# Kernel tuning notes

Hardware: AMD Instinct MI355X
Metric: run time of the kernel (lower is better)

The kernel has to match this reference:

```python
import jax, jax.numpy as jnp
import numpy as np
import math

CHANNELS = 512
OUT_CHANNELS = 512
N_HEADS = 8
WINDOW = 4
K_CH = CHANNELS // N_HEADS


def _conv1x1(x, W, b):
    # x: (B, C_in, T), W: (C_out, C_in), b: (C_out,)
    return jnp.einsum('oc,bct->bot', W, x) + b[None, :, None]


def _get_relative_embeddings(emb, length, window=WINDOW):
    # emb: (H, 2*window+1, k_ch) -> (H, 2*length-1, k_ch)
    pad_length = max(length - (window + 1), 0)
    start = max(window + 1 - length, 0)
    e = jnp.pad(emb, ((0, 0), (pad_length, pad_length), (0, 0))) if pad_length > 0 else emb
    return e[:, start:start + 2 * length - 1]


def _relative_to_absolute(x):
    # x: (B, H, L, 2L-1) -> (B, H, L, L)
    b, h, L, _ = x.shape
    x = jnp.pad(x, ((0, 0), (0, 0), (0, 0), (0, 1)))          # (B,H,L,2L)
    xf = x.reshape(b, h, L * 2 * L)
    xf = jnp.pad(xf, ((0, 0), (0, 0), (L - 1, 0)))
    return xf.reshape(b, h, L + 1, 2 * L - 1)[:, :, :L, L - 1:]


def _absolute_to_relative(x):
    # x: (B, H, L, L) -> (B, H, L, 2L-1)
    b, h, L, _ = x.shape
    x = jnp.pad(x, ((0, 0), (0, 0), (0, 0), (0, L - 1)))       # (B,H,L,2L-1)
    xf = x.reshape(b, h, L * (2 * L - 1))
    xf = jnp.pad(xf, ((0, 0), (0, 0), (L, 0)))
    return xf.reshape(b, h, L, 2 * L)[:, :, :, 1:]


def setup_inputs() -> dict:
    key = jax.random.key(0)
    ks = jax.random.split(key, 16)
    B, C, T = 4, CHANNELS, 1024
    xavier = math.sqrt(2.0 / (C + C))
    rel_std = K_CH ** -0.5
    return {
        'x_q': jax.random.normal(ks[0], (B, C, T), jnp.float32),
        'x_k': jax.random.normal(ks[1], (B, C, T), jnp.float32),
        'x_v': jax.random.normal(ks[2], (B, C, T), jnp.float32),
        'Wq': jax.random.normal(ks[3], (C, C), jnp.float32) * xavier,
        'bq': jnp.zeros((C,), jnp.float32),
        'Wk': jax.random.normal(ks[4], (C, C), jnp.float32) * xavier,
        'bk': jnp.zeros((C,), jnp.float32),
        'Wv': jax.random.normal(ks[5], (C, C), jnp.float32) * xavier,
        'bv': jnp.zeros((C,), jnp.float32),
        'Wo': jax.random.normal(ks[6], (OUT_CHANNELS, C), jnp.float32) * xavier,
        'bo': jnp.zeros((OUT_CHANNELS,), jnp.float32),
        'emb_rel_k': jax.random.normal(ks[7], (N_HEADS, 2 * WINDOW + 1, K_CH), jnp.float32) * rel_std,
        'emb_rel_v': jax.random.normal(ks[8], (N_HEADS, 2 * WINDOW + 1, K_CH), jnp.float32) * rel_std,
    }


def reference(x_q, x_k, x_v, Wq, bq, Wk, bk, Wv, bv, Wo, bo, emb_rel_k, emb_rel_v):
    q = _conv1x1(x_q, Wq, bq)
    k = _conv1x1(x_k, Wk, bk)
    v = _conv1x1(x_v, Wv, bv)
    B, C, T = q.shape
    # (B, C, T) -> (B, H, T, k_ch); head h owns contiguous k_ch channel chunk
    qh = q.reshape(B, N_HEADS, K_CH, T).transpose(0, 1, 3, 2) / math.sqrt(K_CH)
    kh = k.reshape(B, N_HEADS, K_CH, T).transpose(0, 1, 3, 2)
    vh = v.reshape(B, N_HEADS, K_CH, T).transpose(0, 1, 3, 2)
    scores = jnp.einsum('bhtd,bhsd->bhts', qh, kh)              # (B,H,T,T)
    rel_k = _get_relative_embeddings(emb_rel_k, T)              # (H,2T-1,d)
    rel_logits = jnp.einsum('bhtd,hmd->bhtm', qh, rel_k)        # (B,H,T,2T-1)
    scores = scores + _relative_to_absolute(rel_logits)
    attn = jax.nn.softmax(scores, axis=-1)
    ctx = jnp.einsum('bhts,bhsd->bhtd', attn, vh)
    rel_w = _absolute_to_relative(attn)                         # (B,H,T,2T-1)
    rel_v = _get_relative_embeddings(emb_rel_v, T)
    ctx = ctx + jnp.einsum('bhtm,hmd->bhtd', rel_w, rel_v)
    out = ctx.transpose(0, 1, 3, 2).reshape(B, C, T)
    return _conv1x1(out, Wo, bo)
```

## Files before the change

kernel.cpp:

```cpp
#include <hip/hip_runtime.h>

#define T_LEN 1024
#define NH 8
#define DH 64
#define CCH 512
#define LOG2E 1.44269504088896340736f

typedef _Float16 f16;
typedef _Float16 f16x8 __attribute__((ext_vector_type(8)));
typedef _Float16 f16x4 __attribute__((ext_vector_type(4)));
typedef float f32x4 __attribute__((ext_vector_type(4)));

__device__ __forceinline__ void dma16(const void* g, void* l)
{
    __builtin_amdgcn_global_load_lds((const __attribute__((address_space(1))) void*)g,
                                     (__attribute__((address_space(3))) void*)l, 16, 0, 0);
}

__global__ __launch_bounds__(256)
void prep_kernel(const float* __restrict__ x0, const float* __restrict__ x1,
                 const float* __restrict__ x2, const float* __restrict__ W0,
                 const float* __restrict__ W1, const float* __restrict__ W2,
                 const float* __restrict__ W3, f16* __restrict__ o0,
                 f16* __restrict__ o1, f16* __restrict__ o2, f16* __restrict__ w0,
                 f16* __restrict__ w1, f16* __restrict__ w2, f16* __restrict__ w3,
                 int B)
{
    const int z = blockIdx.z;
    if (z < 3 * B) {
        const int t0 = blockIdx.x * 64, c0 = blockIdx.y * 64;
        const int which = z / B, b = z % B;
        const float* x = (which == 0) ? x0 : (which == 1) ? x1 : x2;
        f16* o = (which == 0) ? o0 : (which == 1) ? o1 : o2;

        __shared__ float L[64 * 68];
        const int cl = threadIdx.x & 63, g = threadIdx.x >> 6;
        const float* src = x + ((size_t)(b * CCH + c0 + cl)) * T_LEN + t0 + g * 16;
        #pragma unroll
        for (int j = 0; j < 4; ++j)
            *(float4*)&L[cl * 68 + g * 16 + 4 * j] = *(const float4*)&src[4 * j];
        __syncthreads();
        const int tl = threadIdx.x & 63, cg = (threadIdx.x >> 6) * 16;
        f16 h[16];
        #pragma unroll
        for (int j = 0; j < 16; ++j) h[j] = (f16)L[(cg + j) * 68 + tl];
        f16* dst = o + ((size_t)(b * T_LEN + t0 + tl)) * CCH + c0 + cg;
        *(f16x8*)&dst[0] = *(f16x8*)&h[0];
        *(f16x8*)&dst[8] = *(f16x8*)&h[8];
    } else {
        const int slice = z - 3 * B;
        size_t i = ((size_t)(slice * 128 + blockIdx.y * 16 + blockIdx.x) * 256 + threadIdx.x) * 4;
        const int wi = (int)(i >> 18);
        const size_t off = i & 262143;
        const float* src = (wi == 0) ? W0 : (wi == 1) ? W1 : (wi == 2) ? W2 : W3;
        f16* dst = (wi == 0) ? w0 : (wi == 1) ? w1 : (wi == 2) ? w2 : w3;
        float4 v4 = *(const float4*)&src[off];
        f16x4 h = {(f16)v4.x, (f16)v4.y, (f16)v4.z, (f16)v4.w};
        *(f16x4*)&dst[off] = h;
    }
}

__global__ __launch_bounds__(256)
void proj_qkv(const f16* __restrict__ xq, const f16* __restrict__ xk,
              const f16* __restrict__ xv, const f16* __restrict__ wq,
              const f16* __restrict__ wk, const f16* __restrict__ wv,
              const float* __restrict__ bq, const float* __restrict__ bk,
              const float* __restrict__ bv, f16* __restrict__ qo,
              f16* __restrict__ ko, f16* __restrict__ vo)
{
    const int which = blockIdx.z;
    const f16* X = (which == 0) ? xq : (which == 1) ? xk : xv;
    const f16* W = (which == 0) ? wq : (which == 1) ? wk : wv;
    const float* bias = (which == 0) ? bq : (which == 1) ? bk : bv;
    const float scale = (which == 0) ? 0.125f * LOG2E : 1.0f;

    const int r0 = blockIdx.x * 64;
    const int o0 = blockIdx.y * 64;
    const int tid = threadIdx.x;
    const int w = tid >> 6, quad = (tid >> 4) & 3, l15 = tid & 15;

    __shared__ f16 Xs[64 * 72], Ws[64 * 72];
    f32x4 acc[4] = {};

    for (int c0 = 0; c0 < CCH; c0 += 64) {
        if (c0) __syncthreads();
        #pragma unroll
        for (int j = 0; j < 2; ++j) {
            int cid = tid + 256 * j;
            int row = cid >> 3, c8 = (cid & 7) * 8;
            *(f16x8*)&Xs[row * 72 + c8] = *(const f16x8*)&X[(size_t)(r0 + row) * CCH + c0 + c8];
            *(f16x8*)&Ws[row * 72 + c8] = *(const f16x8*)&W[(size_t)(o0 + row) * CCH + c0 + c8];
        }
        __syncthreads();
        const f16* Ab = (which < 2) ? Xs : Ws;
        const f16* Bb = (which < 2) ? Ws : Xs;
        #pragma unroll
        for (int ks = 0; ks < 2; ++ks) {
            f16x8 a = *(const f16x8*)&Ab[(16 * w + l15) * 72 + ks * 32 + quad * 8];
            #pragma unroll
            for (int ct = 0; ct < 4; ++ct) {
                f16x8 bf = *(const f16x8*)&Bb[(16 * ct + l15) * 72 + ks * 32 + quad * 8];
                acc[ct] = __builtin_amdgcn_mfma_f32_16x16x32_f16(a, bf, acc[ct], 0, 0, 0);
            }
        }
    }

    if (which < 2) {
        f16* out = (which == 0) ? qo : ko;
        #pragma unroll
        for (int ct = 0; ct < 4; ++ct) {
            int col = o0 + 16 * ct + l15;
            float bvl = bias[col];
            #pragma unroll
            for (int r = 0; r < 4; ++r) {
                int row = r0 + 16 * w + quad * 4 + r;
                out[(size_t)row * CCH + col] = (f16)((acc[ct][r] + bvl) * scale);
            }
        }
    } else {
        const int bb = r0 >> 10, tb = r0 & 1023;
        #pragma unroll
        for (int r = 0; r < 4; ++r) {
            int row_o = o0 + 16 * w + quad * 4 + r;
            float bvl = bias[row_o];
            #pragma unroll
            for (int ct = 0; ct < 4; ++ct)
                vo[((size_t)(bb * CCH + row_o)) * T_LEN + tb + 16 * ct + l15] =
                    (f16)(acc[ct][r] + bvl);
        }
    }
}

__global__ __launch_bounds__(256)
void attn_mfma(const f16* __restrict__ q, const f16* __restrict__ kk,
               const f16* __restrict__ v, const float* __restrict__ ekg,
               const float* __restrict__ evg, f16* __restrict__ Op0,
               f16* __restrict__ Op1, float* __restrict__ l0,
               float* __restrict__ l1)
{
    const int t0 = blockIdx.x * 64, h = blockIdx.y;
    const int b = blockIdx.z >> 1, split = blockIdx.z & 1;
    const int tid = threadIdx.x;
    const int w = tid >> 6, lane = tid & 63;
    const int quad = lane >> 4, l15 = lane & 15;

    f16* Op = split ? Op1 : Op0;
    float* lbuf = split ? l1 : l0;

    __shared__ __align__(16) f16 Qs[4096], Ks[4096], Vs[4096], Ps[4096];
    __shared__ float eks[576], evs[576];

    const int srow = tid >> 3;
    const int scol = ((tid & 7) ^ (srow & 7)) << 3;

    for (int i = tid; i < 576; i += 256) {
        eks[i] = ekg[h * 576 + i];
        evs[i] = evg[h * 576 + i];
    }

    dma16(q + ((size_t)(b * T_LEN + t0 + srow)) * CCH + h * DH + scol, &Qs[(size_t)tid * 8]);
    dma16(q + ((size_t)(b * T_LEN + t0 + srow + 32)) * CCH + h * DH + scol, &Qs[((size_t)tid + 256) * 8]);
    __syncthreads();

    f16x8 qf[2];
    #pragma unroll
    for (int ks = 0; ks < 2; ++ks)
        qf[ks] = *(const f16x8*)&Qs[(16 * w + l15) * 64 + (((ks * 4 + quad) ^ (l15 & 7)) << 3)];

    const int kb0 = split * 8;
    const f16* gk = kk + ((size_t)(b * T_LEN + kb0 * 64 + srow)) * CCH + h * DH + scol;
    const f16* gv = v + ((size_t)(b * CCH + h * DH + srow)) * T_LEN + kb0 * 64 + scol;

    const int myt = 16 * w + l15;
    float Ssum = 0.f;
    f32x4 O[4] = {};

    const bool corner_hi = (blockIdx.x == 0) && (split == 1);
    const bool corner_lo = (blockIdx.x == 15) && (split == 0);

    for (int kb = kb0; kb < kb0 + 8; ++kb) {
        __syncthreads();
        dma16(gk, &Ks[(size_t)tid * 8]);
        dma16(gk + (size_t)32 * CCH, &Ks[((size_t)tid + 256) * 8]);
        dma16(gv, &Vs[(size_t)tid * 8]);
        dma16(gv + (size_t)32 * T_LEN, &Vs[((size_t)tid + 256) * 8]);
        gk += (size_t)64 * CCH;
        gv += 64;
        __syncthreads();

        f32x4 S[4] = {};
        #pragma unroll
        for (int ks = 0; ks < 2; ++ks) {
            #pragma unroll
            for (int ct = 0; ct < 4; ++ct) {
                f16x8 a = *(const f16x8*)&Ks[(16 * ct + l15) * 64 + (((ks * 4 + quad) ^ (l15 & 7)) << 3)];
                S[ct] = __builtin_amdgcn_mfma_f32_16x16x32_f16(a, qf[ks], S[ct], 0, 0, 0);
            }
        }

        if ((corner_hi && kb == 15) || (corner_lo && kb == 0)) {
            const int s0g = kb * 64;
            #pragma unroll
            for (int ct = 0; ct < 4; ++ct)
                #pragma unroll
                for (int r = 0; r < 4; ++r) {
                    int t_g = t0 + myt;
                    int s_g = s0g + 16 * ct + 4 * quad + r;
                    int df = s_g - t_g;
                    if (df >= 1019 && df <= 1023) {
                        const float* ekp = &eks[(df - 1019) * 64];
                        float sacc = 0.f;
                        for (int d = 0; d < 64; ++d)
                            sacc += (float)Qs[myt * 64 + (((d >> 3) ^ (myt & 7)) << 3) + (d & 7)] * ekp[d];
                        S[ct][r] += sacc;
                    } else if (df >= -1023 && df <= -1021) {
                        const float* ekp = &eks[(1029 + df) * 64];
                        const int t2 = myt - 1;
                        float sacc = 0.f;
                        for (int d = 0; d < 64; ++d)
                            sacc += (float)Qs[t2 * 64 + (((d >> 3) ^ (t2 & 7)) << 3) + (d & 7)] * ekp[d];
                        S[ct][r] += sacc;
                    }
                }
        }

        #pragma unroll
        for (int ct = 0; ct < 4; ++ct) {
            f16x4 pk_;
            #pragma unroll
            for (int r = 0; r < 4; ++r) {
                float p = exp2f(S[ct][r]);
                Ssum += p;
                pk_[r] = (f16)p;
            }
            int colh = (((2 * ct + (quad >> 1)) ^ (myt & 7)) << 3) + (quad & 1) * 4;
            *(f16x4*)&Ps[myt * 64 + colh] = pk_;
        }
        __syncthreads();

        #pragma unroll
        for (int ks = 0; ks < 2; ++ks) {
            f16x8 a = *(const f16x8*)&Ps[(16 * w + l15) * 64 + (((ks * 4 + quad) ^ (l15 & 7)) << 3)];
            #pragma unroll
            for (int ct = 0; ct < 4; ++ct) {
                f16x8 bf = *(const f16x8*)&Vs[(16 * ct + l15) * 64 + (((ks * 4 + quad) ^ (l15 & 7)) << 3)];
                O[ct] = __builtin_amdgcn_mfma_f32_16x16x32_f16(a, bf, O[ct], 0, 0, 0);
            }
        }

        const int s0g = kb * 64;
        if (s0g <= t0 + 67 && s0g + 63 >= t0 - 4) {
            #pragma unroll
            for (int r = 0; r < 4; ++r) {
                int t_loc = 16 * w + 4 * quad + r;
                int t_g = t0 + t_loc;
                int slo = max(s0g, t_g - 4), shi = min(s0g + 63, t_g + 4);
                for (int s = slo; s <= shi; ++s) {
                    int sl = s - s0g;
                    float p = (float)Ps[t_loc * 64 + (((sl >> 3) ^ (t_loc & 7)) << 3) + (sl & 7)];
                    const float* evp = &evs[(s - t_g + 4) * 64];
                    #pragma unroll
                    for (int ct = 0; ct < 4; ++ct)
                        O[ct][r] += p * evp[16 * ct + l15];
                }
            }
        }
    }

    Ssum += __shfl_xor(Ssum, 16);
    Ssum += __shfl_xor(Ssum, 32);
    if (quad == 0)
        lbuf[((size_t)b * NH + h) * T_LEN + t0 + myt] = Ssum;

    #pragma unroll
    for (int r = 0; r < 4; ++r) {
        int t_g = t0 + 16 * w + 4 * quad + r;
        size_t rowo = ((size_t)(b * T_LEN + t_g)) * CCH + h * DH;
        #pragma unroll
        for (int ct = 0; ct < 4; ++ct)
            Op[rowo + 16 * ct + l15] = (f16)O[ct][r];
    }
}

__global__ __launch_bounds__(256)
void proj_out(const f16* __restrict__ Op0, const f16* __restrict__ Op1,
              const float* __restrict__ l0, const float* __restrict__ l1,
              const f16* __restrict__ Wo, const float* __restrict__ bo,
              float* __restrict__ out)
{
    const int r0 = blockIdx.x * 64;
    const int o0 = blockIdx.y * 64;
    const int tid = threadIdx.x;
    const int w = tid >> 6, quad = (tid >> 4) & 3, l15 = tid & 15;

    __shared__ f16 Xs[64 * 72], Ws[64 * 72];
    f32x4 acc[4] = {};

    for (int c0 = 0; c0 < CCH; c0 += 64) {
        if (c0) __syncthreads();
        #pragma unroll
        for (int j = 0; j < 2; ++j) {
            int cid = tid + 256 * j;
            int rw = cid >> 3, cc = (cid & 7) * 8;
            int gr = r0 + rw;
            int bb = gr >> 10, tt = gr & 1023;
            int hh = (c0 + cc) >> 6;
            size_t li = ((size_t)bb * NH + hh) * T_LEN + tt;
            float rl = 1.0f / (l0[li] + l1[li]);
            f16x8 a0 = *(const f16x8*)&Op0[(size_t)gr * CCH + c0 + cc];
            f16x8 a1 = *(const f16x8*)&Op1[(size_t)gr * CCH + c0 + cc];
            f16 hx[8];
            #pragma unroll
            for (int e = 0; e < 8; ++e)
                hx[e] = (f16)(((float)a0[e] + (float)a1[e]) * rl);
            *(f16x8*)&Xs[rw * 72 + cc] = *(f16x8*)hx;
            *(f16x8*)&Ws[rw * 72 + cc] = *(const f16x8*)&Wo[(size_t)(o0 + rw) * CCH + c0 + cc];
        }
        __syncthreads();
        #pragma unroll
        for (int ks = 0; ks < 2; ++ks) {
            f16x8 a = *(const f16x8*)&Ws[(16 * w + l15) * 72 + ks * 32 + quad * 8];
            #pragma unroll
            for (int ct = 0; ct < 4; ++ct) {
                f16x8 bf = *(const f16x8*)&Xs[(16 * ct + l15) * 72 + ks * 32 + quad * 8];
                acc[ct] = __builtin_amdgcn_mfma_f32_16x16x32_f16(a, bf, acc[ct], 0, 0, 0);
            }
        }
    }

    const int bb = r0 >> 10, tb = r0 & 1023;
    #pragma unroll
    for (int r = 0; r < 4; ++r) {
        int row_o = o0 + 16 * w + quad * 4 + r;
        float bvl = bo[row_o];
        #pragma unroll
        for (int ct = 0; ct < 4; ++ct)
            out[((size_t)(bb * CCH + row_o)) * T_LEN + tb + 16 * ct + l15] =
                acc[ct][r] + bvl;
    }
}

extern "C" void kernel_launch(void* const* d_in, const int* in_sizes, int n_in,
                              void* d_out, int out_size, void* d_ws, size_t ws_size,
                              hipStream_t stream)
{
    const float* x_q = (const float*)d_in[0];
    const float* x_k = (const float*)d_in[1];
    const float* x_v = (const float*)d_in[2];
    const float* Wq  = (const float*)d_in[3];
    const float* bq  = (const float*)d_in[4];
    const float* Wk  = (const float*)d_in[5];
    const float* bk  = (const float*)d_in[6];
    const float* Wv  = (const float*)d_in[7];
    const float* bv  = (const float*)d_in[8];
    const float* Wo  = (const float*)d_in[9];
    const float* bo  = (const float*)d_in[10];
    const float* erk = (const float*)d_in[11];
    const float* erv = (const float*)d_in[12];

    const int B = in_sizes[0] / (CCH * T_LEN);
    const size_t te = (size_t)B * CCH * T_LEN;
    const size_t we = (size_t)CCH * CCH;

    f16* p = (f16*)d_ws;
    f16* xTq = p; p += te;
    f16* xTk = p; p += te;
    f16* xTv = p; p += te;
    f16* wqh = p; p += we;
    f16* wkh = p; p += we;
    f16* wvh = p; p += we;
    f16* woh = p; p += we;
    f16* qh  = p; p += te;
    f16* kh  = p; p += te;
    f16* vh  = p; p += te;

    f16* Op0 = xTq;
    f16* Op1 = xTk;
    float* l0 = (float*)xTv;
    float* l1 = l0 + (size_t)B * NH * T_LEN;

    dim3 blk(256);
    prep_kernel<<<dim3(16, 8, 3 * B + 8), blk, 0, stream>>>(
        x_q, x_k, x_v, Wq, Wk, Wv, Wo, xTq, xTk, xTv, wqh, wkh, wvh, woh, B);
    proj_qkv<<<dim3(B * 16, 8, 3), blk, 0, stream>>>(
        xTq, xTk, xTv, wqh, wkh, wvh, bq, bk, bv, qh, kh, vh);
    attn_mfma<<<dim3(T_LEN / 64, NH, 2 * B), blk, 0, stream>>>(
        qh, kh, vh, erk, erv, Op0, Op1, l0, l1);
    proj_out<<<dim3(B * 16, 8), blk, 0, stream>>>(
        Op0, Op1, l0, l1, woh, bo, (float*)d_out);
}
```

Baseline: 166.4 us.

## Double-buffer projection GEMMs with async LDS DMA, swizzle, and split combine kernel

Both projection GEMMs move to 128x64 tiles with double-buffered shared memory filled by global_load_lds DMA and an XOR swizzle in place of padding, so the next K-chunk loads while MFMAs run. The split-softmax combine (sum of the two partial outputs and normalisation) moves out of proj_out into its own elementwise kernel that writes a normalised context buffer, which lets proj_out use plain DMA loads. This adds one launch and an extra read/write of the context tensor, plus new workspace buffers instead of reusing the input scratch. Doubling the rows per tile halves the grid, which may reduce occupancy.

After: 159.8 us. -4.0%, faster.

```diff
diff --git a/kernel.cpp b/kernel.cpp
--- a/kernel.cpp
+++ b/kernel.cpp
@@ -74,59 +74,99 @@
     const float* bias = (which == 0) ? bq : (which == 1) ? bk : bv;
     const float scale = (which == 0) ? 0.125f * LOG2E : 1.0f;
 
-    const int r0 = blockIdx.x * 64;
+    const int r0 = blockIdx.x * 128;
     const int o0 = blockIdx.y * 64;
     const int tid = threadIdx.x;
-    const int w = tid >> 6, quad = (tid >> 4) & 3, l15 = tid & 15;
-
-    __shared__ f16 Xs[64 * 72], Ws[64 * 72];
-    f32x4 acc[4] = {};
-
-    for (int c0 = 0; c0 < CCH; c0 += 64) {
-        if (c0) __syncthreads();
-        #pragma unroll
-        for (int j = 0; j < 2; ++j) {
-            int cid = tid + 256 * j;
-            int row = cid >> 3, c8 = (cid & 7) * 8;
-            *(f16x8*)&Xs[row * 72 + c8] = *(const f16x8*)&X[(size_t)(r0 + row) * CCH + c0 + c8];
-            *(f16x8*)&Ws[row * 72 + c8] = *(const f16x8*)&W[(size_t)(o0 + row) * CCH + c0 + c8];
-        }
-        __syncthreads();
-        const f16* Ab = (which < 2) ? Xs : Ws;
-        const f16* Bb = (which < 2) ? Ws : Xs;
+    const int w = tid >> 6, lane = tid & 63;
+    const int quad = lane >> 4, l15 = lane & 15;
+
+    __shared__ __align__(16) f16 Xs[2][128 * 64];
+    __shared__ __align__(16) f16 Ws[2][64 * 64];
+
+    const int srow = tid >> 3;
+    const int scol = ((tid & 7) ^ (srow & 7)) << 3;
+
+    const f16* Xg = X + (size_t)(r0 + srow) * CCH + scol;
+    const f16* Wg = W + (size_t)(o0 + srow) * CCH + scol;
+
+    #pragma unroll
+    for (int j = 0; j < 4; ++j)
+        dma16(Xg + (size_t)(32 * j) * CCH, &Xs[0][(size_t)tid * 8 + j * 2048]);
+    #pragma unroll
+    for (int j = 0; j < 2; ++j)
+        dma16(Wg + (size_t)(32 * j) * CCH, &Ws[0][(size_t)tid * 8 + j * 2048]);
+
+    f32x4 acc[8] = {};
+
+    for (int kc = 0; kc < 8; ++kc) {
+        __syncthreads();
+        if (kc < 7) {
+            const int bf = (kc + 1) & 1, c1 = (kc + 1) * 64;
+            #pragma unroll
+            for (int j = 0; j < 4; ++j)
+                dma16(Xg + c1 + (size_t)(32 * j) * CCH, &Xs[bf][(size_t)tid * 8 + j * 2048]);
+            #pragma unroll
+            for (int j = 0; j < 2; ++j)
+                dma16(Wg + c1 + (size_t)(32 * j) * CCH, &Ws[bf][(size_t)tid * 8 + j * 2048]);
+        }
+        const int cb = kc & 1;
         #pragma unroll
         for (int ks = 0; ks < 2; ++ks) {
-            f16x8 a = *(const f16x8*)&Ab[(16 * w + l15) * 72 + ks * 32 + quad * 8];
-            #pragma unroll
-            for (int ct = 0; ct < 4; ++ct) {
-                f16x8 bf = *(const f16x8*)&Bb[(16 * ct + l15) * 72 + ks * 32 + quad * 8];
-                acc[ct] = __builtin_amdgcn_mfma_f32_16x16x32_f16(a, bf, acc[ct], 0, 0, 0);
+            const int sl = ((ks * 4 + quad) ^ (l15 & 7)) << 3;
+            f16x8 xf[2], wf[4];
+            #pragma unroll
+            for (int im = 0; im < 2; ++im)
+                xf[im] = *(const f16x8*)&Xs[cb][(32 * w + 16 * im + l15) * 64 + sl];
+            #pragma unroll
+            for (int cm = 0; cm < 4; ++cm)
+                wf[cm] = *(const f16x8*)&Ws[cb][(16 * cm + l15) * 64 + sl];
+            if (which < 2) {
+                #pragma unroll
+                for (int im = 0; im < 2; ++im)
+                    #pragma unroll
+                    for (int cm = 0; cm < 4; ++cm)
+                        acc[im * 4 + cm] = __builtin_amdgcn_mfma_f32_16x16x32_f16(
+                            xf[im], wf[cm], acc[im * 4 + cm], 0, 0, 0);
+            } else {
+                #pragma unroll
+                for (int cm = 0; cm < 4; ++cm)
+                    #pragma unroll
+                    for (int in = 0; in < 2; ++in)
+                        acc[cm * 2 + in] = __builtin_amdgcn_mfma_f32_16x16x32_f16(
+                            wf[cm], xf[in], acc[cm * 2 + in], 0, 0, 0);
             }
         }
     }
 
     if (which < 2) {
         f16* out = (which == 0) ? qo : ko;
-        #pragma unroll
-        for (int ct = 0; ct < 4; ++ct) {
-            int col = o0 + 16 * ct + l15;
-            float bvl = bias[col];
+        float bl[4];
+        #pragma unroll
+        for (int cm = 0; cm < 4; ++cm) bl[cm] = bias[o0 + 16 * cm + l15];
+        #pragma unroll
+        for (int im = 0; im < 2; ++im)
             #pragma unroll
             for (int r = 0; r < 4; ++r) {
-                int row = r0 + 16 * w + quad * 4 + r;
-                out[(size_t)row * CCH + col] = (f16)((acc[ct][r] + bvl) * scale);
-            }
-        }
+                size_t row = (size_t)(r0 + 32 * w + 16 * im + 4 * quad + r) * CCH;
+                #pragma unroll
+                for (int cm = 0; cm < 4; ++cm)
+                    out[row + o0 + 16 * cm + l15] =
+                        (f16)((acc[im * 4 + cm][r] + bl[cm]) * scale);
+            }
     } else {
         const int bb = r0 >> 10, tb = r0 & 1023;
         #pragma unroll
-        for (int r = 0; r < 4; ++r) {
-            int row_o = o0 + 16 * w + quad * 4 + r;
-            float bvl = bias[row_o];
-            #pragma unroll
-            for (int ct = 0; ct < 4; ++ct)
-                vo[((size_t)(bb * CCH + row_o)) * T_LEN + tb + 16 * ct + l15] =
-                    (f16)(acc[ct][r] + bvl);
+        for (int cm = 0; cm < 4; ++cm) {
+            float4 bv4 = *(const float4*)&bias[o0 + 16 * cm + 4 * quad];
+            float bl[4] = {bv4.x, bv4.y, bv4.z, bv4.w};
+            #pragma unroll
+            for (int r = 0; r < 4; ++r) {
+                size_t row = ((size_t)(bb * CCH + o0 + 16 * cm + 4 * quad + r)) * T_LEN;
+                #pragma unroll
+                for (int in = 0; in < 2; ++in)
+                    vo[row + tb + 32 * w + 16 * in + l15] =
+                        (f16)(acc[cm * 2 + in][r] + bl[r]);
+            }
         }
     }
 }
@@ -283,60 +323,95 @@
 }
 
 __global__ __launch_bounds__(256)
-void proj_out(const f16* __restrict__ Op0, const f16* __restrict__ Op1,
-              const float* __restrict__ l0, const float* __restrict__ l1,
-              const f16* __restrict__ Wo, const float* __restrict__ bo,
-              float* __restrict__ out)
-{
-    const int r0 = blockIdx.x * 64;
+void combine_kernel(const f16* __restrict__ Op0, const f16* __restrict__ Op1,
+                    const float* __restrict__ l0, const float* __restrict__ l1,
+                    f16* __restrict__ ctx)
+{
+    const size_t i8 = ((size_t)blockIdx.x * 256 + threadIdx.x) * 8;
+    const size_t gr = i8 >> 9;
+    const int h = (int)((i8 & 511) >> 6);
+    const size_t li = ((gr >> 10) * NH + h) * T_LEN + (gr & 1023);
+    const float rl = 1.0f / (l0[li] + l1[li]);
+    f16x8 a0 = *(const f16x8*)&Op0[i8];
+    f16x8 a1 = *(const f16x8*)&Op1[i8];
+    f16 o[8];
+    #pragma unroll
+    for (int e = 0; e < 8; ++e)
+        o[e] = (f16)(((float)a0[e] + (float)a1[e]) * rl);
+    *(f16x8*)&ctx[i8] = *(f16x8*)o;
+}
+
+__global__ __launch_bounds__(256)
+void proj_out(const f16* __restrict__ ctx, const f16* __restrict__ Wo,
+              const float* __restrict__ bo, float* __restrict__ out)
+{
+    const int r0 = blockIdx.x * 128;
     const int o0 = blockIdx.y * 64;
     const int tid = threadIdx.x;
-    const int w = tid >> 6, quad = (tid >> 4) & 3, l15 = tid & 15;
-
-    __shared__ f16 Xs[64 * 72], Ws[64 * 72];
-    f32x4 acc[4] = {};
-
-    for (int c0 = 0; c0 < CCH; c0 += 64) {
-        if (c0) __syncthreads();
-        #pragma unroll
-        for (int j = 0; j < 2; ++j) {
-            int cid = tid + 256 * j;
-            int rw = cid >> 3, cc = (cid & 7) * 8;
-            int gr = r0 + rw;
-            int bb = gr >> 10, tt = gr & 1023;
-            int hh = (c0 + cc) >> 6;
-            size_t li = ((size_t)bb * NH + hh) * T_LEN + tt;
-            float rl = 1.0f / (l0[li] + l1[li]);
-            f16x8 a0 = *(const f16x8*)&Op0[(size_t)gr * CCH + c0 + cc];
-            f16x8 a1 = *(const f16x8*)&Op1[(size_t)gr * CCH + c0 + cc];
-            f16 hx[8];
-            #pragma unroll
-            for (int e = 0; e < 8; ++e)
-                hx[e] = (f16)(((float)a0[e] + (float)a1[e]) * rl);
-            *(f16x8*)&Xs[rw * 72 + cc] = *(f16x8*)hx;
-            *(f16x8*)&Ws[rw * 72 + cc] = *(const f16x8*)&Wo[(size_t)(o0 + rw) * CCH + c0 + cc];
-        }
-        __syncthreads();
+    const int w = tid >> 6, lane = tid & 63;
+    const int quad = lane >> 4, l15 = lane & 15;
+
+    __shared__ __align__(16) f16 Cs[2][128 * 64];
+    __shared__ __align__(16) f16 Ws[2][64 * 64];
+
+    const int srow = tid >> 3;
+    const int scol = ((tid & 7) ^ (srow & 7)) << 3;
+
+    const f16* Cg = ctx + (size_t)(r0 + srow) * CCH + scol;
+    const f16* Wg = Wo + (size_t)(o0 + srow) * CCH + scol;
+
+    #pragma unroll
+    for (int j = 0; j < 4; ++j)
+        dma16(Cg + (size_t)(32 * j) * CCH, &Cs[0][(size_t)tid * 8 + j * 2048]);
+    #pragma unroll
+    for (int j = 0; j < 2; ++j)
+        dma16(Wg + (size_t)(32 * j) * CCH, &Ws[0][(size_t)tid * 8 + j * 2048]);
+
+    f32x4 acc[8] = {};
+
+    for (int kc = 0; kc < 8; ++kc) {
+        __syncthreads();
+        if (kc < 7) {
+            const int bf = (kc + 1) & 1, c1 = (kc + 1) * 64;
+            #pragma unroll
+            for (int j = 0; j < 4; ++j)
+                dma16(Cg + c1 + (size_t)(32 * j) * CCH, &Cs[bf][(size_t)tid * 8 + j * 2048]);
+            #pragma unroll
+            for (int j = 0; j < 2; ++j)
+                dma16(Wg + c1 + (size_t)(32 * j) * CCH, &Ws[bf][(size_t)tid * 8 + j * 2048]);
+        }
+        const int cb = kc & 1;
         #pragma unroll
         for (int ks = 0; ks < 2; ++ks) {
-            f16x8 a = *(const f16x8*)&Ws[(16 * w + l15) * 72 + ks * 32 + quad * 8];
-            #pragma unroll
-            for (int ct = 0; ct < 4; ++ct) {
-                f16x8 bf = *(const f16x8*)&Xs[(16 * ct + l15) * 72 + ks * 32 + quad * 8];
-                acc[ct] = __builtin_amdgcn_mfma_f32_16x16x32_f16(a, bf, acc[ct], 0, 0, 0);
-            }
+            const int sl = ((ks * 4 + quad) ^ (l15 & 7)) << 3;
+            f16x8 cf[2], wf[4];
+            #pragma unroll
+            for (int in = 0; in < 2; ++in)
+                cf[in] = *(const f16x8*)&Cs[cb][(32 * w + 16 * in + l15) * 64 + sl];
+            #pragma unroll
+            for (int cm = 0; cm < 4; ++cm)
+                wf[cm] = *(const f16x8*)&Ws[cb][(16 * cm + l15) * 64 + sl];
+            #pragma unroll
+            for (int cm = 0; cm < 4; ++cm)
+                #pragma unroll
+                for (int in = 0; in < 2; ++in)
+                    acc[cm * 2 + in] = __builtin_amdgcn_mfma_f32_16x16x32_f16(
+                        wf[cm], cf[in], acc[cm * 2 + in], 0, 0, 0);
         }
     }
 
     const int bb = r0 >> 10, tb = r0 & 1023;
     #pragma unroll
-    for (int r = 0; r < 4; ++r) {
-        int row_o = o0 + 16 * w + quad * 4 + r;
-        float bvl = bo[row_o];
-        #pragma unroll
-        for (int ct = 0; ct < 4; ++ct)
-            out[((size_t)(bb * CCH + row_o)) * T_LEN + tb + 16 * ct + l15] =
-                acc[ct][r] + bvl;
+    for (int cm = 0; cm < 4; ++cm) {
+        float4 bv4 = *(const float4*)&bo[o0 + 16 * cm + 4 * quad];
+        float bl[4] = {bv4.x, bv4.y, bv4.z, bv4.w};
+        #pragma unroll
+        for (int r = 0; r < 4; ++r) {
+            size_t row = ((size_t)(bb * CCH + o0 + 16 * cm + 4 * quad + r)) * T_LEN;
+            #pragma unroll
+            for (int in = 0; in < 2; ++in)
+                out[row + tb + 32 * w + 16 * in + l15] = acc[cm * 2 + in][r] + bl[r];
+        }
     }
 }
 
@@ -373,19 +448,19 @@
     f16* qh  = p; p += te;
     f16* kh  = p; p += te;
     f16* vh  = p; p += te;
-
-    f16* Op0 = xTq;
-    f16* Op1 = xTk;
-    float* l0 = (float*)xTv;
+    f16* Op0 = p; p += te;
+    f16* Op1 = p; p += te;
+    f16* ch  = p; p += te;
+    float* l0 = (float*)p;
     float* l1 = l0 + (size_t)B * NH * T_LEN;
 
     dim3 blk(256);
     prep_kernel<<<dim3(16, 8, 3 * B + 8), blk, 0, stream>>>(
         x_q, x_k, x_v, Wq, Wk, Wv, Wo, xTq, xTk, xTv, wqh, wkh, wvh, woh, B);
-    proj_qkv<<<dim3(B * 16, 8, 3), blk, 0, stream>>>(
+    proj_qkv<<<dim3(B * 8, 8, 3), blk, 0, stream>>>(
         xTq, xTk, xTv, wqh, wkh, wvh, bq, bk, bv, qh, kh, vh);
     attn_mfma<<<dim3(T_LEN / 64, NH, 2 * B), blk, 0, stream>>>(
         qh, kh, vh, erk, erv, Op0, Op1, l0, l1);
-    proj_out<<<dim3(B * 16, 8), blk, 0, stream>>>(
-        Op0, Op1, l0, l1, woh, bo, (float*)d_out);
-}
+    combine_kernel<<<dim3(B * 256), blk, 0, stream>>>(Op0, Op1, l0, l1, ch);
+    proj_out<<<dim3(B * 8, 8), blk, 0, stream>>>(ch, woh, bo, (float*)d_out);
+}
```
